# Kernel tuning notes

Measured on AMD Instinct MI355X. Metric: run time of the kernel, lower is better.

Reference implementation:

```python
import jax, jax.numpy as jnp
import numpy as np
import math

S, D, H, HD = 2048, 1280, 16, 80  # seq_len, embed_dim, num_heads, head_dim


def setup_inputs() -> dict:
    key = jax.random.key(0)
    k1, k2, k3, k4, k5, k6 = jax.random.split(key, 6)
    hidden_states = jax.random.normal(k1, (S, D), dtype=jnp.float32)
    # 4 equal-length segments (e.g. 4 images of 512 patches)
    cu_seqlens = jnp.array([0, 512, 1024, 1536, 2048], dtype=jnp.int32)
    # RoPE theta*position angles, [S, HD//2]
    rotary_pos_emb = jax.random.uniform(k2, (S, HD // 2), dtype=jnp.float32) * 10.0
    qkv_w = jax.random.normal(k3, (3 * D, D), dtype=jnp.float32) * 0.02
    qkv_b = jax.random.normal(k4, (3 * D,), dtype=jnp.float32) * 0.02
    proj_w = jax.random.normal(k5, (D, D), dtype=jnp.float32) * 0.02
    proj_b = jax.random.normal(k6, (D,), dtype=jnp.float32) * 0.02
    return {"hidden_states": hidden_states, "cu_seqlens": cu_seqlens,
            "rotary_pos_emb": rotary_pos_emb, "qkv_w": qkv_w, "qkv_b": qkv_b,
            "proj_w": proj_w, "proj_b": proj_b}


def _rotate_half(x):
    x1, x2 = jnp.split(x, 2, axis=-1)
    return jnp.concatenate([-x2, x1], axis=-1)


def _square_mask(n, seq, dtype):
    # faithful translation of rewrite_loop_for_square_mask on a full-min mask
    neg = jnp.finfo(dtype).min
    mask = jnp.full((1, n, n), neg, dtype=dtype)
    r = jnp.arange(n)
    less0 = (r[:, None] < seq[None, :]).astype(jnp.int32)
    less = less0.sum(axis=-1, keepdims=True) + 1            # [n,1] segment label
    sq = less * less.T                                       # [n,n]
    c1 = jnp.logical_or(seq.min() == 0, less != less.max())
    c2 = jnp.logical_or(seq.max() == n, less != less.min())
    look = (c1 & c2).astype(jnp.int32) * less
    filt = (sq != look ** 2).astype(dtype)                   # 0 inside blocks, 1 outside
    return mask * filt


def reference(hidden_states, cu_seqlens, rotary_pos_emb, qkv_w, qkv_b, proj_w, proj_b):
    seq_len = hidden_states.shape[0]
    qkv = hidden_states @ qkv_w.T + qkv_b                    # [S, 3D]
    qkv = qkv.reshape(seq_len, 3, H, HD)
    q, k, v = qkv[:, 0], qkv[:, 1], qkv[:, 2]                # [S, H, HD]

    # rotary_pos_emb path: emb = cat(rope, rope), cos/sin broadcast over heads
    emb = jnp.concatenate([rotary_pos_emb, rotary_pos_emb], axis=-1)  # [S, HD]
    cos = jnp.cos(emb)[:, None, :]                           # [S, 1, HD]
    sin = jnp.sin(emb)[:, None, :]
    q = q * cos + _rotate_half(q) * sin
    k = k * cos + _rotate_half(k) * sin

    mask = _square_mask(seq_len, cu_seqlens, q.dtype)        # [1, S, S]

    qh = q.transpose(1, 0, 2)                                # [H, S, HD]
    kh = k.transpose(1, 0, 2)
    vh = v.transpose(1, 0, 2)

    attn = jnp.einsum('hqd,hkd->hqk', qh, kh) / math.sqrt(HD)  # [H, S, S]
    attn = attn + mask
    attn = jax.nn.softmax(attn.astype(jnp.float32), axis=-1).astype(q.dtype)
    out = jnp.einsum('hqk,hkd->hqd', attn, vh)               # [H, S, HD]
    out = out.transpose(1, 0, 2).reshape(seq_len, -1)        # [S, D]
    return out @ proj_w.T + proj_b
```

## Files before the change

### kernel.cpp

```cpp
#include <hip/hip_runtime.h>


typedef unsigned short u16;
typedef short short8 __attribute__((ext_vector_type(8)));
typedef float floatx4 __attribute__((ext_vector_type(4)));
typedef u16 ushort4v __attribute__((ext_vector_type(4)));
typedef float float4v __attribute__((ext_vector_type(4)));

#define S_LEN 2048
#define DMODEL 1280
#define NHEAD 16
#define HDIM 80
#define HDIM_P 96
#define SEGS 4
#define SEG_LEN 512
#define QSCALE 0.11180339887498948f

__device__ __forceinline__ float b2f(u16 u) {
  union { unsigned int i; float f; } v; v.i = ((unsigned int)u) << 16; return v.f;
}
__device__ __forceinline__ u16 f2b(float f) {
  union { float f; unsigned int i; } v; v.f = f;
  unsigned int i = v.i;
  return (u16)((i + 0x7FFFu + ((i >> 16) & 1u)) >> 16);
}

__device__ __forceinline__ void load_lds16(const u16* g, u16* l) {
  __builtin_amdgcn_global_load_lds(
      (const __attribute__((address_space(1))) unsigned int*)g,
      (__attribute__((address_space(3))) unsigned int*)l, 16, 0, 0);
}

__device__ __forceinline__ unsigned int rope_perm(unsigned int j) {
  if (j >= 2560u) return j;
  unsigned int sec = j / 1280u;
  unsigned int jj = j - sec * 1280u;
  unsigned int h = jj / 80u, d = jj - h * 80u;
  unsigned int dp = (d < 40u) ? (2u * d) : (2u * (d - 40u) + 1u);
  return sec * 1280u + h * 80u + dp;
}

__global__ __launch_bounds__(256) void convert_all(
    const void* __restrict__ s_hid, const void* __restrict__ s_qw,
    const void* __restrict__ s_pw,  const void* __restrict__ s_rope,
    const void* __restrict__ s_qb,  const void* __restrict__ s_pb,
    u16* __restrict__ d_hid, u16* __restrict__ d_qw, u16* __restrict__ d_pw,
    u16* __restrict__ d_rope, u16* __restrict__ d_qb, u16* __restrict__ d_pb,
    int* __restrict__ flag_out, float* __restrict__ cs_tab,
    float* __restrict__ sn_tab) {
  unsigned int w = ((const unsigned int*)s_rope)[threadIdx.x & 63];
  int is_f32 = __any((int)((w >> 15) & 1));
  if (blockIdx.x == 0 && threadIdx.x == 0) *flag_out = is_f32;

  unsigned int qi = blockIdx.x * 256 + threadIdx.x;

  if (qi >= 2315520u) {
    unsigned int ti = qi - 2315520u;
    float ang = is_f32 ? ((const float*)s_rope)[ti]
                       : b2f(((const u16*)s_rope)[ti]);
    cs_tab[ti] = cosf(ang);
    sn_tab[ti] = sinf(ang);
    return;
  }

  if (qi >= 2314240u && qi < 2315200u) {
    unsigned int off = qi - 2314240u;
    ushort4v o;
    if (is_f32) {
      float4v f = ((const float4v*)s_qb)[off];
      #pragma unroll
      for (int i = 0; i < 4; ++i) o[i] = f2b(f[i]);
    } else {
      o = ((const ushort4v*)s_qb)[off];
    }
    #pragma unroll
    for (int e = 0; e < 4; ++e) d_qb[rope_perm(off * 4u + e)] = o[e];
    return;
  }

  const void* src; u16* dst; unsigned int off, doff;
  if      (qi < 655360u)  { src = s_hid;  dst = d_hid;  off = qi;            doff = off; }
  else if (qi < 1884160u) {
    src = s_qw; dst = d_qw; off = qi - 655360u;
    unsigned int row = off / 320u, col = off - row * 320u;
    doff = rope_perm(row) * 320u + col;
  }
  else if (qi < 2293760u) { src = s_pw;   dst = d_pw;   off = qi - 1884160u; doff = off; }
  else if (qi < 2314240u) { src = s_rope; dst = d_rope; off = qi - 2293760u; doff = off; }
  else                    { src = s_pb;   dst = d_pb;   off = qi - 2315200u; doff = off; }
  ushort4v o;
  if (is_f32) {
    float4v f = ((const float4v*)src)[off];
    #pragma unroll
    for (int i = 0; i < 4; ++i) o[i] = f2b(f[i]);
  } else {
    o = ((const ushort4v*)src)[off];
  }
  ((ushort4v*)dst)[doff] = o;
}

__global__ __launch_bounds__(256) void gemm_qkv(
    const u16* __restrict__ A, const u16* __restrict__ W,
    const u16* __restrict__ bias,
    u16* __restrict__ qh, u16* __restrict__ kh, u16* __restrict__ vt,
    const float* __restrict__ cs, const float* __restrict__ sn) {
  const int K = DMODEL;
  __shared__ __attribute__((aligned(16))) u16 As[2][128 * 64];
  __shared__ __attribute__((aligned(16))) u16 Bs[2][128 * 64];
  int wave = threadIdx.x >> 6, lane = threadIdx.x & 63;
  int r = lane & 15, q = lane >> 4;
  int wm = wave >> 1, wn = wave & 1;
  int m0 = blockIdx.y * 128, n0 = blockIdx.x * 128;

  int srow = lane >> 3;
  int sg   = (lane & 7) ^ srow;
  const u16* Ab = A + (size_t)(m0 + srow) * K + sg * 8;
  const u16* Wb = W + (size_t)(n0 + srow) * K + sg * 8;

  floatx4 acc[4][4];
  #pragma unroll
  for (int mi = 0; mi < 4; ++mi)
    #pragma unroll
    for (int ni = 0; ni < 4; ++ni) acc[mi][ni] = (floatx4){0.f, 0.f, 0.f, 0.f};

  #pragma unroll
  for (int c = 0; c < 4; ++c) {
    int ch = wave * 4 + c;
    load_lds16(Ab + (size_t)(ch * 8) * K, &As[0][ch * 8 * 64]);
    load_lds16(Wb + (size_t)(ch * 8) * K, &Bs[0][ch * 8 * 64]);
  }
  int buf = 0;
  for (int kt = 0; kt < K; kt += 64, buf ^= 1) {
    __syncthreads();
    if (kt + 64 < K) {
      #pragma unroll
      for (int c = 0; c < 4; ++c) {
        int ch = wave * 4 + c;
        load_lds16(Ab + kt + 64 + (size_t)(ch * 8) * K, &As[buf ^ 1][ch * 8 * 64]);
        load_lds16(Wb + kt + 64 + (size_t)(ch * 8) * K, &Bs[buf ^ 1][ch * 8 * 64]);
      }
    }
    #pragma unroll
    for (int ks = 0; ks < 2; ++ks) {
      short8 af[4], bf[4];
      #pragma unroll
      for (int i = 0; i < 4; ++i) {
        int arow = wm * 64 + i * 16 + r;
        int brow = wn * 64 + i * 16 + r;
        af[i] = *(const short8*)&As[buf][arow * 64 + (((ks * 4 + q) ^ (arow & 7)) * 8)];
        bf[i] = *(const short8*)&Bs[buf][brow * 64 + (((ks * 4 + q) ^ (brow & 7)) * 8)];
      }
      #pragma unroll
      for (int mi = 0; mi < 4; ++mi)
        #pragma unroll
        for (int ni = 0; ni < 4; ++ni)
          acc[mi][ni] = __builtin_amdgcn_mfma_f32_16x16x32_bf16(af[mi], bf[ni],
                                                                acc[mi][ni], 0, 0, 0);
    }
  }

  #pragma unroll
  for (int ni = 0; ni < 4; ++ni) {
    int col = n0 + wn * 64 + ni * 16 + r;
    float bv = b2f(bias[col]);
    if (col < 2 * DMODEL) {
      int isq = col < DMODEL;
      int c2 = isq ? col : col - DMODEL;
      int h = c2 / HDIM, cin = c2 % HDIM;
      int idx = cin >> 1;
      int odd = cin & 1;
      float scale = isq ? QSCALE : 1.0f;
      u16* dst = (isq ? qh : kh) + (size_t)h * S_LEN * HDIM_P + cin;
      #pragma unroll
      for (int mi = 0; mi < 4; ++mi) {
        int row0 = m0 + wm * 64 + mi * 16 + q * 4;
        #pragma unroll
        for (int i = 0; i < 4; ++i) {
          float a = acc[mi][ni][i] + bv;
          float b = __shfl_xor(a, 1);
          int s = row0 + i;
          float cc = cs[s * 40 + idx], ss = sn[s * 40 + idx];
          float v = odd ? (a * cc + b * ss) : (a * cc - b * ss);
          dst[(size_t)s * HDIM_P] = f2b(v * scale);
        }
      }
    } else {
      int c2 = col - 2 * DMODEL;
      #pragma unroll
      for (int mi = 0; mi < 4; ++mi) {
        int row0 = m0 + wm * 64 + mi * 16 + q * 4;
        ushort4v pk;
        #pragma unroll
        for (int i = 0; i < 4; ++i) pk[i] = f2b(acc[mi][ni][i] + bv);
        *(ushort4v*)(vt + (size_t)c2 * S_LEN + row0) = pk;
      }
    }
  }
}

#define PPAD 136
#define OPAD 84
struct WaveScratch {
  union {
    u16   P[32][PPAD];
    float O[32][OPAD];
  };
};
__global__ __launch_bounds__(256) void flash_attn(
    const u16* __restrict__ qh, const u16* __restrict__ kh,
    const u16* __restrict__ vt, const int* __restrict__ cu,
    u16* __restrict__ attn_out) {
  __shared__ __attribute__((aligned(16))) WaveScratch wsc[4];
  int wave = threadIdx.x >> 6, lane = threadIdx.x & 63;
  int r = lane & 15, q = lane >> 4;
  int hz = blockIdx.x;
  int seg = hz & (SEGS - 1), h = hz >> 2;
  int base = cu[seg];
  int m0 = blockIdx.y * 32;
  int k0 = wave * 128;

  const short8 zero8 = {0, 0, 0, 0, 0, 0, 0, 0};
  const u16* Qrow0 = qh + ((size_t)h * S_LEN + base + m0 + r) * HDIM_P + q * 8;
  const u16* Qrow1 = Qrow0 + (size_t)16 * HDIM_P;
  short8 aq[2][3];
  aq[0][0] = *(const short8*)(Qrow0);
  aq[0][1] = *(const short8*)(Qrow0 + 32);
  aq[0][2] = (q < 2) ? *(const short8*)(Qrow0 + 64) : zero8;
  aq[1][0] = *(const short8*)(Qrow1);
  aq[1][1] = *(const short8*)(Qrow1 + 32);
  aq[1][2] = (q < 2) ? *(const short8*)(Qrow1 + 64) : zero8;

  const u16* Kb = kh + ((size_t)h * S_LEN + base + k0 + r) * HDIM_P + q * 8;
  const u16* Vb = vt + ((size_t)h * HDIM + r) * S_LEN + base + k0 + q * 8;

  floatx4 sacc[2][8];
  #pragma unroll
  for (int g = 0; g < 8; ++g) {
    const u16* Kg = Kb + (size_t)(16 * g) * HDIM_P;
    short8 kf0 = *(const short8*)(Kg);
    short8 kf1 = *(const short8*)(Kg + 32);
    short8 kf2 = (q < 2) ? *(const short8*)(Kg + 64) : zero8;
    #pragma unroll
    for (int t = 0; t < 2; ++t) {
      floatx4 s = {0.f, 0.f, 0.f, 0.f};
      s = __builtin_amdgcn_mfma_f32_16x16x32_bf16(aq[t][0], kf0, s, 0, 0, 0);
      s = __builtin_amdgcn_mfma_f32_16x16x32_bf16(aq[t][1], kf1, s, 0, 0, 0);
      s = __builtin_amdgcn_mfma_f32_16x16x32_bf16(aq[t][2], kf2, s, 0, 0, 0);
      sacc[t][g] = s;
    }
  }

  #pragma unroll
  for (int t = 0; t < 2; ++t)
    #pragma unroll
    for (int g = 0; g < 8; ++g)
      #pragma unroll
      for (int i = 0; i < 4; ++i)
        wsc[wave].P[t * 16 + q * 4 + i][g * 16 + r] = f2b(__expf(sacc[t][g][i]));

  floatx4 o[2][5], o5[2];
  #pragma unroll
  for (int t = 0; t < 2; ++t) {
    o5[t] = (floatx4){0.f, 0.f, 0.f, 0.f};
    #pragma unroll
    for (int t5 = 0; t5 < 5; ++t5) o[t][t5] = (floatx4){0.f, 0.f, 0.f, 0.f};
  }
  const short8 ones = {0x3F80, 0x3F80, 0x3F80, 0x3F80, 0x3F80, 0x3F80, 0x3F80, 0x3F80};
  #pragma unroll
  for (int kq = 0; kq < 4; ++kq) {
    short8 pa0 = *(const short8*)&wsc[wave].P[r][kq * 32 + q * 8];
    short8 pa1 = *(const short8*)&wsc[wave].P[16 + r][kq * 32 + q * 8];
    #pragma unroll
    for (int t5 = 0; t5 < 5; ++t5) {
      short8 bv = *(const short8*)(Vb + kq * 32 + (size_t)(t5 * 16) * S_LEN);
      o[0][t5] = __builtin_amdgcn_mfma_f32_16x16x32_bf16(pa0, bv, o[0][t5], 0, 0, 0);
      o[1][t5] = __builtin_amdgcn_mfma_f32_16x16x32_bf16(pa1, bv, o[1][t5], 0, 0, 0);
    }
    o5[0] = __builtin_amdgcn_mfma_f32_16x16x32_bf16(pa0, ones, o5[0], 0, 0, 0);
    o5[1] = __builtin_amdgcn_mfma_f32_16x16x32_bf16(pa1, ones, o5[1], 0, 0, 0);
  }
  #pragma unroll
  for (int t = 0; t < 2; ++t)
    #pragma unroll
    for (int t5 = 0; t5 < 5; ++t5)
      #pragma unroll
      for (int i = 0; i < 4; ++i)
        wsc[wave].O[t * 16 + q * 4 + i][t5 * 16 + r] = o[t][t5][i];
  if (r == 0) {
    #pragma unroll
    for (int t = 0; t < 2; ++t)
      #pragma unroll
      for (int i = 0; i < 4; ++i) wsc[wave].O[t * 16 + q * 4 + i][80] = o5[t][i];
  }
  __syncthreads();

  int tid = threadIdx.x;
  int row = tid >> 3;
  int c0 = (tid & 7) * 10;
  float L = wsc[0].O[row][80] + wsc[1].O[row][80] +
            wsc[2].O[row][80] + wsc[3].O[row][80];
  float invL = 1.0f / L;
  u16* Or = attn_out + (size_t)(base + m0 + row) * DMODEL + h * HDIM + c0;
  #pragma unroll
  for (int j = 0; j < 10; ++j) {
    float v = wsc[0].O[row][c0 + j] + wsc[1].O[row][c0 + j] +
              wsc[2].O[row][c0 + j] + wsc[3].O[row][c0 + j];
    Or[j] = f2b(v * invL);
  }
}

__global__ __launch_bounds__(256) void gemm_tiled(
    const u16* __restrict__ A, const u16* __restrict__ W,
    const u16* __restrict__ bias, void* __restrict__ C,
    int M, int N, int K, const int* __restrict__ out_flag) {
  __shared__ __attribute__((aligned(16))) u16 As[2][64 * 64];
  __shared__ __attribute__((aligned(16))) u16 Bs[2][128 * 64];
  int wave = threadIdx.x >> 6, lane = threadIdx.x & 63;
  int r = lane & 15, q = lane >> 4;
  int wm = wave >> 1, wn = wave & 1;
  int m0 = blockIdx.y * 64, n0 = blockIdx.x * 128;

  int srow = lane >> 3;
  int sg   = (lane & 7) ^ srow;
  const u16* Ab = A + (size_t)(m0 + srow) * K + sg * 8;
  const u16* Wb = W + (size_t)(n0 + srow) * K + sg * 8;

  floatx4 acc[2][4];
  #pragma unroll
  for (int mi = 0; mi < 2; ++mi)
    #pragma unroll
    for (int ni = 0; ni < 4; ++ni) acc[mi][ni] = (floatx4){0.f, 0.f, 0.f, 0.f};

  #pragma unroll
  for (int c = 0; c < 2; ++c)
    load_lds16(Ab + (size_t)((wave * 2 + c) * 8) * K, &As[0][(wave * 2 + c) * 8 * 64]);
  #pragma unroll
  for (int c = 0; c < 4; ++c)
    load_lds16(Wb + (size_t)((wave * 4 + c) * 8) * K, &Bs[0][(wave * 4 + c) * 8 * 64]);

  int buf = 0;
  for (int kt = 0; kt < K; kt += 64, buf ^= 1) {
    __syncthreads();
    if (kt + 64 < K) {
      #pragma unroll
      for (int c = 0; c < 2; ++c)
        load_lds16(Ab + kt + 64 + (size_t)((wave * 2 + c) * 8) * K,
                   &As[buf ^ 1][(wave * 2 + c) * 8 * 64]);
      #pragma unroll
      for (int c = 0; c < 4; ++c)
        load_lds16(Wb + kt + 64 + (size_t)((wave * 4 + c) * 8) * K,
                   &Bs[buf ^ 1][(wave * 4 + c) * 8 * 64]);
    }
    #pragma unroll
    for (int ks = 0; ks < 2; ++ks) {
      short8 af[2], bf[4];
      #pragma unroll
      for (int i = 0; i < 2; ++i) {
        int arow = wm * 32 + i * 16 + r;
        af[i] = *(const short8*)&As[buf][arow * 64 + (((ks * 4 + q) ^ (arow & 7)) * 8)];
      }
      #pragma unroll
      for (int i = 0; i < 4; ++i) {
        int brow = wn * 64 + i * 16 + r;
        bf[i] = *(const short8*)&Bs[buf][brow * 64 + (((ks * 4 + q) ^ (brow & 7)) * 8)];
      }
      #pragma unroll
      for (int mi = 0; mi < 2; ++mi)
        #pragma unroll
        for (int ni = 0; ni < 4; ++ni)
          acc[mi][ni] = __builtin_amdgcn_mfma_f32_16x16x32_bf16(af[mi], bf[ni],
                                                                acc[mi][ni], 0, 0, 0);
    }
  }

  int f32out = out_flag ? *out_flag : 0;
  #pragma unroll
  for (int ni = 0; ni < 4; ++ni) {
    int col = n0 + wn * 64 + ni * 16 + r;
    float bv = b2f(bias[col]);
    #pragma unroll
    for (int mi = 0; mi < 2; ++mi) {
      size_t row0 = (size_t)(m0 + wm * 32 + mi * 16 + q * 4);
      if (f32out) {
        float* out = (float*)C;
        #pragma unroll
        for (int i = 0; i < 4; ++i) out[(row0 + i) * N + col] = acc[mi][ni][i] + bv;
      } else {
        u16* out = (u16*)C;
        #pragma unroll
        for (int i = 0; i < 4; ++i) out[(row0 + i) * N + col] = f2b(acc[mi][ni][i] + bv);
      }
    }
  }
}

extern "C" void kernel_launch(void* const* d_in, const int* in_sizes, int n_in,
                              void* d_out, int out_size, void* d_ws, size_t ws_size,
                              hipStream_t stream) {
  const void* hidden_r = d_in[0];
  const int*  cu       = (const int*)d_in[1];
  const void* rope_r   = d_in[2];
  const void* qkv_w_r  = d_in[3];
  const void* qkv_b_r  = d_in[4];
  const void* proj_w_r = d_in[5];
  const void* proj_b_r = d_in[6];

  char* ws = (char*)d_ws;
  u16* hidden_c = (u16*)(ws);
  u16* qkvw_c   = (u16*)(ws +  6291456u);
  u16* projw_c  = (u16*)(ws + 16777216u);
  u16* rope_c   = (u16*)(ws + 20971520u);
  u16* qkvb_c   = (u16*)(ws + 21135360u);
  u16* projb_c  = (u16*)(ws + 21143040u);
  int* flag     = (int*)(ws + 21145600u);
  float* cs_tab = (float*)(ws + 22020096u);
  float* sn_tab = (float*)(ws + 22347776u);
  u16* qh       = (u16*)(ws + 25165824u);
  u16* kh       = (u16*)(ws + 31457280u);
  u16* vt       = (u16*)(ws + 37748736u);
  u16* attn_out = (u16*)(ws + 44040192u);

  convert_all<<<dim3(9365), dim3(256), 0, stream>>>(
      hidden_r, qkv_w_r, proj_w_r, rope_r, qkv_b_r, proj_b_r,
      hidden_c, qkvw_c, projw_c, rope_c, qkvb_c, projb_c, flag, cs_tab, sn_tab);

  gemm_qkv<<<dim3(3840 / 128, 2048 / 128), dim3(256), 0, stream>>>(
      hidden_c, qkvw_c, qkvb_c, qh, kh, vt, cs_tab, sn_tab);

  flash_attn<<<dim3(NHEAD * SEGS, SEG_LEN / 32), dim3(256), 0, stream>>>(
      qh, kh, vt, cu, attn_out);

  gemm_tiled<<<dim3(1280 / 128, 2048 / 64), dim3(256), 0, stream>>>(
      attn_out, projw_c, projb_c, d_out, S_LEN, DMODEL, DMODEL, flag);
}
```

Before: 163.9 us.

## Stage QKV GEMM epilogue through LDS for vectorized RoPE and V stores

The QKV GEMM epilogue now writes the bias-added accumulator tile into shared memory, reusing the A/B staging buffers. It then reads back contiguous 8-element chunks per thread to apply RoPE with vector cos/sin loads and emits 16-byte stores for Q/K, plus a transposed tile for V. This replaces scattered 2-byte global stores and per-element shuffles with coalesced writes, at the cost of an extra LDS round trip, two barriers and an intermediate bf16 rounding before the rotation. The unused bf16 copy of the rope angles is also dropped from the conversion kernel, shrinking its grid.

```diff
diff --git a/kernel.cpp b/kernel.cpp
--- a/kernel.cpp
+++ b/kernel.cpp
@@ -45,7 +45,7 @@
     const void* __restrict__ s_pw,  const void* __restrict__ s_rope,
     const void* __restrict__ s_qb,  const void* __restrict__ s_pb,
     u16* __restrict__ d_hid, u16* __restrict__ d_qw, u16* __restrict__ d_pw,
-    u16* __restrict__ d_rope, u16* __restrict__ d_qb, u16* __restrict__ d_pb,
+    u16* __restrict__ d_qb, u16* __restrict__ d_pb,
     int* __restrict__ flag_out, float* __restrict__ cs_tab,
     float* __restrict__ sn_tab) {
   unsigned int w = ((const unsigned int*)s_rope)[threadIdx.x & 63];
@@ -54,8 +54,8 @@
 
   unsigned int qi = blockIdx.x * 256 + threadIdx.x;
 
-  if (qi >= 2315520u) {
-    unsigned int ti = qi - 2315520u;
+  if (qi >= 2295040u) {
+    unsigned int ti = qi - 2295040u;
     float ang = is_f32 ? ((const float*)s_rope)[ti]
                        : b2f(((const u16*)s_rope)[ti]);
     cs_tab[ti] = cosf(ang);
@@ -63,8 +63,8 @@
     return;
   }
 
-  if (qi >= 2314240u && qi < 2315200u) {
-    unsigned int off = qi - 2314240u;
+  if (qi >= 2293760u && qi < 2294720u) {
+    unsigned int off = qi - 2293760u;
     ushort4v o;
     if (is_f32) {
       float4v f = ((const float4v*)s_qb)[off];
@@ -86,8 +86,7 @@
     doff = rope_perm(row) * 320u + col;
   }
   else if (qi < 2293760u) { src = s_pw;   dst = d_pw;   off = qi - 1884160u; doff = off; }
-  else if (qi < 2314240u) { src = s_rope; dst = d_rope; off = qi - 2293760u; doff = off; }
-  else                    { src = s_pb;   dst = d_pb;   off = qi - 2315200u; doff = off; }
+  else                    { src = s_pb;   dst = d_pb;   off = qi - 2294720u; doff = off; }
   ushort4v o;
   if (is_f32) {
     float4v f = ((const float4v*)src)[off];
@@ -105,8 +104,9 @@
     u16* __restrict__ qh, u16* __restrict__ kh, u16* __restrict__ vt,
     const float* __restrict__ cs, const float* __restrict__ sn) {
   const int K = DMODEL;
-  __shared__ __attribute__((aligned(16))) u16 As[2][128 * 64];
-  __shared__ __attribute__((aligned(16))) u16 Bs[2][128 * 64];
+  __shared__ __attribute__((aligned(16))) u16 smem[4 * 128 * 64];
+  u16 (*As)[128 * 64] = (u16(*)[128 * 64])(smem);
+  u16 (*Bs)[128 * 64] = (u16(*)[128 * 64])(smem + 2 * 128 * 64);
   int wave = threadIdx.x >> 6, lane = threadIdx.x & 63;
   int r = lane & 15, q = lane >> 4;
   int wm = wave >> 1, wn = wave & 1;
@@ -159,41 +159,78 @@
     }
   }
 
-  #pragma unroll
-  for (int ni = 0; ni < 4; ++ni) {
-    int col = n0 + wn * 64 + ni * 16 + r;
-    float bv = b2f(bias[col]);
-    if (col < 2 * DMODEL) {
-      int isq = col < DMODEL;
-      int c2 = isq ? col : col - DMODEL;
-      int h = c2 / HDIM, cin = c2 % HDIM;
-      int idx = cin >> 1;
-      int odd = cin & 1;
-      float scale = isq ? QSCALE : 1.0f;
-      u16* dst = (isq ? qh : kh) + (size_t)h * S_LEN * HDIM_P + cin;
+  __syncthreads();
+  u16 (*L)[136] = (u16(*)[136])smem;
+  int isV = (n0 >= 2 * DMODEL);
+
+  if (!isV) {
+    #pragma unroll
+    for (int ni = 0; ni < 4; ++ni) {
+      int col = wn * 64 + ni * 16 + r;
+      float bv = b2f(bias[n0 + col]);
       #pragma unroll
       for (int mi = 0; mi < 4; ++mi) {
-        int row0 = m0 + wm * 64 + mi * 16 + q * 4;
-        #pragma unroll
-        for (int i = 0; i < 4; ++i) {
-          float a = acc[mi][ni][i] + bv;
-          float b = __shfl_xor(a, 1);
-          int s = row0 + i;
-          float cc = cs[s * 40 + idx], ss = sn[s * 40 + idx];
-          float v = odd ? (a * cc + b * ss) : (a * cc - b * ss);
-          dst[(size_t)s * HDIM_P] = f2b(v * scale);
-        }
-      }
-    } else {
-      int c2 = col - 2 * DMODEL;
+        int row0 = wm * 64 + mi * 16 + q * 4;
+        #pragma unroll
+        for (int i = 0; i < 4; ++i)
+          L[row0 + i][col] = f2b(acc[mi][ni][i] + bv);
+      }
+    }
+  } else {
+    #pragma unroll
+    for (int ni = 0; ni < 4; ++ni) {
+      int col = wn * 64 + ni * 16 + r;
+      float bv = b2f(bias[n0 + col]);
       #pragma unroll
       for (int mi = 0; mi < 4; ++mi) {
-        int row0 = m0 + wm * 64 + mi * 16 + q * 4;
+        int row0 = wm * 64 + mi * 16 + q * 4;
         ushort4v pk;
         #pragma unroll
         for (int i = 0; i < 4; ++i) pk[i] = f2b(acc[mi][ni][i] + bv);
-        *(ushort4v*)(vt + (size_t)c2 * S_LEN + row0) = pk;
-      }
+        *(ushort4v*)&L[col][row0] = pk;
+      }
+    }
+  }
+  __syncthreads();
+
+  int tid = threadIdx.x;
+  if (!isV) {
+    int sl = tid >> 1;
+    int c0 = (tid & 1) * 64;
+    int sg2 = m0 + sl;
+    int isq = n0 < DMODEL;
+    float scale = isq ? QSCALE : 1.0f;
+    int cbase = (isq ? n0 : n0 - DMODEL) + c0;
+    u16* dstbase = isq ? qh : kh;
+    const float* csrow = cs + sg2 * 40;
+    const float* snrow = sn + sg2 * 40;
+    #pragma unroll
+    for (int j = 0; j < 8; ++j) {
+      int c2 = cbase + j * 8;
+      int h = c2 / HDIM;
+      int cin = c2 - h * HDIM;
+      int idx0 = cin >> 1;
+      float4v cs4 = *(const float4v*)(csrow + idx0);
+      float4v sn4 = *(const float4v*)(snrow + idx0);
+      short8 ch = *(const short8*)&L[sl][c0 + j * 8];
+      short8 out;
+      #pragma unroll
+      for (int e = 0; e < 4; ++e) {
+        float a = b2f((u16)ch[2 * e]), b = b2f((u16)ch[2 * e + 1]);
+        out[2 * e]     = (short)f2b((a * cs4[e] - b * sn4[e]) * scale);
+        out[2 * e + 1] = (short)f2b((b * cs4[e] + a * sn4[e]) * scale);
+      }
+      *(short8*)(dstbase + ((size_t)h * S_LEN + sg2) * HDIM_P + cin) = out;
+    }
+  } else {
+    int cl = tid >> 1;
+    int s0 = (tid & 1) * 64;
+    int c2 = (n0 - 2 * DMODEL) + cl;
+    u16* dstc = vt + (size_t)c2 * S_LEN + m0 + s0;
+    #pragma unroll
+    for (int j = 0; j < 8; ++j) {
+      short8 vch = *(const short8*)&L[cl][s0 + j * 8];
+      *(short8*)(dstc + j * 8) = vch;
     }
   }
 }
@@ -409,7 +446,6 @@
   u16* hidden_c = (u16*)(ws);
   u16* qkvw_c   = (u16*)(ws +  6291456u);
   u16* projw_c  = (u16*)(ws + 16777216u);
-  u16* rope_c   = (u16*)(ws + 20971520u);
   u16* qkvb_c   = (u16*)(ws + 21135360u);
   u16* projb_c  = (u16*)(ws + 21143040u);
   int* flag     = (int*)(ws + 21145600u);
@@ -420,9 +456,9 @@
   u16* vt       = (u16*)(ws + 37748736u);
   u16* attn_out = (u16*)(ws + 44040192u);
 
-  convert_all<<<dim3(9365), dim3(256), 0, stream>>>(
+  convert_all<<<dim3(9285), dim3(256), 0, stream>>>(
       hidden_r, qkv_w_r, proj_w_r, rope_r, qkv_b_r, proj_b_r,
-      hidden_c, qkvw_c, projw_c, rope_c, qkvb_c, projb_c, flag, cs_tab, sn_tab);
+      hidden_c, qkvw_c, projw_c, qkvb_c, projb_c, flag, cs_tab, sn_tab);
 
   gemm_qkv<<<dim3(3840 / 128, 2048 / 128), dim3(256), 0, stream>>>(
       hidden_c, qkvw_c, qkvb_c, qh, kh, vt, cs_tab, sn_tab);
```

Measured after the change: 164.9 us. No clear change (+0.6%).

## Swap MFMA operands for Q/K epilogue, remap blocks per XCD, drop unused rope copy

Applied to the files above, without the earlier changes.

For Q/K tiles the QKV GEMM now computes the transposed product, so each lane holds four consecutive output columns. The RoPE pair rotation then happens in registers with vectorized cos/sin loads and 8-byte stores, replacing per-element shuffles and scalar stores. Both GEMMs remap block IDs so that consecutive blocks on the same XCD share row tiles, aiming for better L2 reuse. The unused bf16 rope copy is removed from the conversion kernel, which shrinks its grid.

```diff
diff --git a/kernel.cpp b/kernel.cpp
--- a/kernel.cpp
+++ b/kernel.cpp
@@ -6,6 +6,7 @@
 typedef float floatx4 __attribute__((ext_vector_type(4)));
 typedef u16 ushort4v __attribute__((ext_vector_type(4)));
 typedef float float4v __attribute__((ext_vector_type(4)));
+typedef float float2v __attribute__((ext_vector_type(2)));
 
 #define S_LEN 2048
 #define DMODEL 1280
@@ -45,7 +46,7 @@
     const void* __restrict__ s_pw,  const void* __restrict__ s_rope,
     const void* __restrict__ s_qb,  const void* __restrict__ s_pb,
     u16* __restrict__ d_hid, u16* __restrict__ d_qw, u16* __restrict__ d_pw,
-    u16* __restrict__ d_rope, u16* __restrict__ d_qb, u16* __restrict__ d_pb,
+    u16* __restrict__ d_qb, u16* __restrict__ d_pb,
     int* __restrict__ flag_out, float* __restrict__ cs_tab,
     float* __restrict__ sn_tab) {
   unsigned int w = ((const unsigned int*)s_rope)[threadIdx.x & 63];
@@ -54,8 +55,8 @@
 
   unsigned int qi = blockIdx.x * 256 + threadIdx.x;
 
-  if (qi >= 2315520u) {
-    unsigned int ti = qi - 2315520u;
+  if (qi >= 2295040u) {
+    unsigned int ti = qi - 2295040u;
     float ang = is_f32 ? ((const float*)s_rope)[ti]
                        : b2f(((const u16*)s_rope)[ti]);
     cs_tab[ti] = cosf(ang);
@@ -63,8 +64,8 @@
     return;
   }
 
-  if (qi >= 2314240u && qi < 2315200u) {
-    unsigned int off = qi - 2314240u;
+  if (qi >= 2293760u && qi < 2294720u) {
+    unsigned int off = qi - 2293760u;
     ushort4v o;
     if (is_f32) {
       float4v f = ((const float4v*)s_qb)[off];
@@ -86,8 +87,7 @@
     doff = rope_perm(row) * 320u + col;
   }
   else if (qi < 2293760u) { src = s_pw;   dst = d_pw;   off = qi - 1884160u; doff = off; }
-  else if (qi < 2314240u) { src = s_rope; dst = d_rope; off = qi - 2293760u; doff = off; }
-  else                    { src = s_pb;   dst = d_pb;   off = qi - 2315200u; doff = off; }
+  else                    { src = s_pb;   dst = d_pb;   off = qi - 2294720u; doff = off; }
   ushort4v o;
   if (is_f32) {
     float4v f = ((const float4v*)src)[off];
@@ -110,7 +110,13 @@
   int wave = threadIdx.x >> 6, lane = threadIdx.x & 63;
   int r = lane & 15, q = lane >> 4;
   int wm = wave >> 1, wn = wave & 1;
-  int m0 = blockIdx.y * 128, n0 = blockIdx.x * 128;
+
+  int id = blockIdx.x + 30 * blockIdx.y;
+  int xcd = id & 7, slot = id >> 3;
+  int bx = slot % 30;
+  int by = 2 * xcd + slot / 30;
+  int m0 = by * 128, n0 = bx * 128;
+  const int isV = (n0 >= 2 * DMODEL);
 
   int srow = lane >> 3;
   int sg   = (lane & 7) ^ srow;
@@ -119,9 +125,9 @@
 
   floatx4 acc[4][4];
   #pragma unroll
-  for (int mi = 0; mi < 4; ++mi)
-    #pragma unroll
-    for (int ni = 0; ni < 4; ++ni) acc[mi][ni] = (floatx4){0.f, 0.f, 0.f, 0.f};
+  for (int a = 0; a < 4; ++a)
+    #pragma unroll
+    for (int b = 0; b < 4; ++b) acc[a][b] = (floatx4){0.f, 0.f, 0.f, 0.f};
 
   #pragma unroll
   for (int c = 0; c < 4; ++c) {
@@ -150,41 +156,59 @@
         af[i] = *(const short8*)&As[buf][arow * 64 + (((ks * 4 + q) ^ (arow & 7)) * 8)];
         bf[i] = *(const short8*)&Bs[buf][brow * 64 + (((ks * 4 + q) ^ (brow & 7)) * 8)];
       }
-      #pragma unroll
-      for (int mi = 0; mi < 4; ++mi)
+      if (isV) {
+        #pragma unroll
+        for (int mi = 0; mi < 4; ++mi)
+          #pragma unroll
+          for (int ni = 0; ni < 4; ++ni)
+            acc[mi][ni] = __builtin_amdgcn_mfma_f32_16x16x32_bf16(af[mi], bf[ni],
+                                                                  acc[mi][ni], 0, 0, 0);
+      } else {
         #pragma unroll
         for (int ni = 0; ni < 4; ++ni)
-          acc[mi][ni] = __builtin_amdgcn_mfma_f32_16x16x32_bf16(af[mi], bf[ni],
-                                                                acc[mi][ni], 0, 0, 0);
-    }
-  }
-
-  #pragma unroll
-  for (int ni = 0; ni < 4; ++ni) {
-    int col = n0 + wn * 64 + ni * 16 + r;
-    float bv = b2f(bias[col]);
-    if (col < 2 * DMODEL) {
-      int isq = col < DMODEL;
-      int c2 = isq ? col : col - DMODEL;
-      int h = c2 / HDIM, cin = c2 % HDIM;
-      int idx = cin >> 1;
-      int odd = cin & 1;
+          #pragma unroll
+          for (int mi = 0; mi < 4; ++mi)
+            acc[ni][mi] = __builtin_amdgcn_mfma_f32_16x16x32_bf16(bf[ni], af[mi],
+                                                                  acc[ni][mi], 0, 0, 0);
+      }
+    }
+  }
+
+  if (!isV) {
+    #pragma unroll
+    for (int ni = 0; ni < 4; ++ni) {
+      int fbase = n0 + wn * 64 + ni * 16 + q * 4;
+      int isq = fbase < DMODEL;
+      int c2 = fbase - (isq ? 0 : DMODEL);
+      int h = c2 / HDIM, cin = c2 - h * HDIM;
       float scale = isq ? QSCALE : 1.0f;
-      u16* dst = (isq ? qh : kh) + (size_t)h * S_LEN * HDIM_P + cin;
+      u16* dstb = (isq ? qh : kh) + (size_t)h * S_LEN * HDIM_P + cin;
+      ushort4v bv4 = *(const ushort4v*)&bias[fbase];
+      float b0 = b2f(bv4[0]), b1 = b2f(bv4[1]);
+      float b2v = b2f(bv4[2]), b3 = b2f(bv4[3]);
+      int idx0 = cin >> 1;
       #pragma unroll
       for (int mi = 0; mi < 4; ++mi) {
-        int row0 = m0 + wm * 64 + mi * 16 + q * 4;
-        #pragma unroll
-        for (int i = 0; i < 4; ++i) {
-          float a = acc[mi][ni][i] + bv;
-          float b = __shfl_xor(a, 1);
-          int s = row0 + i;
-          float cc = cs[s * 40 + idx], ss = sn[s * 40 + idx];
-          float v = odd ? (a * cc + b * ss) : (a * cc - b * ss);
-          dst[(size_t)s * HDIM_P] = f2b(v * scale);
-        }
-      }
-    } else {
+        int s = m0 + wm * 64 + mi * 16 + r;
+        float2v c2v = *(const float2v*)(cs + (size_t)s * 40 + idx0);
+        float2v s2v = *(const float2v*)(sn + (size_t)s * 40 + idx0);
+        float a0 = acc[ni][mi][0] + b0;
+        float a1 = acc[ni][mi][1] + b1;
+        float a2 = acc[ni][mi][2] + b2v;
+        float a3 = acc[ni][mi][3] + b3;
+        ushort4v o;
+        o[0] = f2b((a0 * c2v[0] - a1 * s2v[0]) * scale);
+        o[1] = f2b((a1 * c2v[0] + a0 * s2v[0]) * scale);
+        o[2] = f2b((a2 * c2v[1] - a3 * s2v[1]) * scale);
+        o[3] = f2b((a3 * c2v[1] + a2 * s2v[1]) * scale);
+        *(ushort4v*)(dstb + (size_t)s * HDIM_P) = o;
+      }
+    }
+  } else {
+    #pragma unroll
+    for (int ni = 0; ni < 4; ++ni) {
+      int col = n0 + wn * 64 + ni * 16 + r;
+      float bv = b2f(bias[col]);
       int c2 = col - 2 * DMODEL;
       #pragma unroll
       for (int mi = 0; mi < 4; ++mi) {
@@ -318,7 +342,15 @@
   int wave = threadIdx.x >> 6, lane = threadIdx.x & 63;
   int r = lane & 15, q = lane >> 4;
   int wm = wave >> 1, wn = wave & 1;
-  int m0 = blockIdx.y * 64, n0 = blockIdx.x * 128;
+
+  int bx = blockIdx.x, by = blockIdx.y;
+  if (gridDim.x == 10 && gridDim.y == 32) {
+    int id = bx + 10 * by;
+    int xcd = id & 7, slot = id >> 3;
+    bx = slot % 10;
+    by = 4 * xcd + slot / 10;
+  }
+  int m0 = by * 64, n0 = bx * 128;
 
   int srow = lane >> 3;
   int sg   = (lane & 7) ^ srow;
@@ -409,7 +441,6 @@
   u16* hidden_c = (u16*)(ws);
   u16* qkvw_c   = (u16*)(ws +  6291456u);
   u16* projw_c  = (u16*)(ws + 16777216u);
-  u16* rope_c   = (u16*)(ws + 20971520u);
   u16* qkvb_c   = (u16*)(ws + 21135360u);
   u16* projb_c  = (u16*)(ws + 21143040u);
   int* flag     = (int*)(ws + 21145600u);
@@ -420,9 +451,9 @@
   u16* vt       = (u16*)(ws + 37748736u);
   u16* attn_out = (u16*)(ws + 44040192u);
 
-  convert_all<<<dim3(9365), dim3(256), 0, stream>>>(
+  convert_all<<<dim3(9285), dim3(256), 0, stream>>>(
       hidden_r, qkv_w_r, proj_w_r, rope_r, qkv_b_r, proj_b_r,
-      hidden_c, qkvw_c, projw_c, rope_c, qkvb_c, projb_c, flag, cs_tab, sn_tab);
+      hidden_c, qkvw_c, projw_c, qkvb_c, projb_c, flag, cs_tab, sn_tab);
 
   gemm_qkv<<<dim3(3840 / 128, 2048 / 128), dim3(256), 0, stream>>>(
       hidden_c, qkvw_c, qkvb_c, qh, kh, vt, cs_tab, sn_tab);
```

Measured after the change: 162.9 us. Within noise of the previous version (-0.6%).
